# Performance work log

Hardware: AMD Instinct MI355X
Metric: run time of the kernel (lower is better)

Reference implementation:

```python
import jax, jax.numpy as jnp
import numpy as np

NEIGH = 16  # default neigh in __init__


def setup_inputs() -> dict:
    key = jax.random.key(0)
    kx, kuv = jax.random.split(key)
    B, M = 8, 4096
    X = jax.random.normal(kx, (B, M, 3), dtype=jnp.float32)
    uv = jax.random.uniform(kuv, (B, M, 2), dtype=jnp.float32)
    return {"X": X, "uv": uv}


def reference(X, uv):
    # Pairwise squared distances in parameter (uv) space: (B, M, M)
    dm = jnp.sum((uv[:, :, None, :] - uv[:, None, :, :]) ** 2, axis=-1)
    # k nearest neighbours (smallest distances) -> indices (B, M, K)
    _, k_inds = jax.lax.top_k(-dm, NEIGH)
    # Gather 3D neighbourhoods: (B, M, K, 3)
    knns = jax.vmap(lambda x, idx: x[idx])(X, k_inds)
    # Covariance per point: center then K x 3 outer products -> (B, M, 3, 3)
    centered = knns - jnp.mean(knns, axis=2, keepdims=True)
    cov = jnp.einsum('bmki,bmkj->bmij', centered, centered)
    # Symmetric 3x3 eigenvalues; torch sorts descending, eigvalsh is ascending
    eig = jnp.linalg.eigvalsh(cov)
    fff = eig[..., ::-1]  # (B, M, 3), descending
    return fff
```

## Files before the change

kernel.cpp:

```cpp
#include <hip/hip_runtime.h>
#include <hip/hip_bf16.h>
#include <math.h>

typedef unsigned long long u64;
typedef unsigned int u32;
typedef unsigned short u16;

constexpr int NB  = 8;
constexpr int NM  = 4096;
constexpr int KNN = 16;
constexpr int WPB = 8;
constexpr int QPW = 4;
constexpr int QPB = WPB * QPW;
constexpr int BLK = WPB * 64;
constexpr int GC  = 16;
constexpr int NC  = GC * GC;
constexpr int CSST = NC + 1;
constexpr int SLG = 12;
constexpr int SLC = 8;

constexpr size_t WS_UVS = 0;
constexpr size_t WS_IDX = 262144;
constexpr size_t WS_CS  = 327680;

__device__ __forceinline__ u64 shflx64(u64 v, int m) {
  unsigned lo = (unsigned)v, hi = (unsigned)(v >> 32);
  lo = __shfl_xor(lo, m, 64);
  hi = __shfl_xor(hi, m, 64);
  return ((u64)hi << 32) | lo;
}
__device__ __forceinline__ int rfl(int x) { return __builtin_amdgcn_readfirstlane(x); }
__device__ __forceinline__ int lanes_below(u64 m) {
  return (int)__builtin_amdgcn_mbcnt_hi((u32)(m >> 32),
             __builtin_amdgcn_mbcnt_lo((u32)m, 0u));
}
__device__ __forceinline__ u32 gm16(u64 m, int lane) {
  return (u32)(m >> ((lane >> 4) << 4)) & 0xFFFFu;
}

__global__ __launch_bounds__(1024)
void bin_pts(const float* __restrict__ uv, float2* __restrict__ uvS,
             u16* __restrict__ idxS, u32* __restrict__ cs) {
  __shared__ u32 cnt[NC];
  __shared__ u32 offs[NC];
  __shared__ u32 wtot[4];
  const int bb  = blockIdx.x;
  const int tid = threadIdx.x;

  if (tid < NC) cnt[tid] = 0;
  __syncthreads();

  float2 c4[4];
  int cell[4];
  #pragma unroll
  for (int i = 0; i < 4; ++i) {
    const int p = tid + i * 1024;
    const float2 c = ((const float2*)(uv + (size_t)bb * NM * 2))[p];
    int cx = (int)(c.x * (float)GC); cx = cx > GC - 1 ? GC - 1 : (cx < 0 ? 0 : cx);
    int cy = (int)(c.y * (float)GC); cy = cy > GC - 1 ? GC - 1 : (cy < 0 ? 0 : cy);
    c4[i] = c; cell[i] = cy * GC + cx;
    atomicAdd(&cnt[cell[i]], 1u);
  }
  __syncthreads();

  if (tid < NC) {
    const int lane = tid & 63;
    u32 inc = cnt[tid];
    #pragma unroll
    for (int o = 1; o < 64; o <<= 1) {
      const u32 t = __shfl_up(inc, o, 64);
      if (lane >= o) inc += t;
    }
    offs[tid] = inc;
    if (lane == 63) wtot[tid >> 6] = inc;
  }
  __syncthreads();
  if (tid < NC) {
    const int w = tid >> 6;
    u32 base = 0;
    #pragma unroll
    for (int i = 0; i < 3; ++i) base += (i < w) ? wtot[i] : 0;
    const u32 excl = base + offs[tid] - cnt[tid];
    cs[bb * CSST + tid] = excl;
    offs[tid] = excl;
    if (tid == 0) cs[bb * CSST + NC] = NM;
  }
  __syncthreads();

  #pragma unroll
  for (int i = 0; i < 4; ++i) {
    const int p = tid + i * 1024;
    const u32 pos = atomicAdd(&offs[cell[i]], 1u);
    uvS[(size_t)bb * NM + pos]  = c4[i];
    idxS[(size_t)bb * NM + pos] = (u16)p;
  }
}

__global__ __launch_bounds__(BLK, 8)
void knn_eig(const float* __restrict__ X, const float* __restrict__ uv,
             const float2* __restrict__ uvS, const u16* __restrict__ idxS,
             const u32* __restrict__ cs, float* __restrict__ out) {
  __shared__ u64 surv[WPB][QPW * 32];

  const int tid  = threadIdx.x;
  const int lane = tid & 63;
  const int sub  = lane & 15;
  const int g4   = lane >> 4;
  const int wv   = tid >> 6;
  const int bb   = blockIdx.x >> 7;
  const int q    = ((blockIdx.x & 127) << 5) + (wv << 2) + g4;

  const float qu = uv[((size_t)bb * NM + q) * 2];
  const float qv = uv[((size_t)bb * NM + q) * 2 + 1];
  int cxv = (int)(qu * (float)GC); cxv = cxv > GC - 1 ? GC - 1 : (cxv < 0 ? 0 : cxv);
  int cyv = (int)(qv * (float)GC); cyv = cyv > GC - 1 ? GC - 1 : (cyv < 0 ? 0 : cyv);
  const u32* csb = cs + bb * CSST;
  const float2* uvb = uvS + (size_t)bb * NM;
  const u16* idxb = idxS + (size_t)bb * NM;

  float d[SLG];
  #pragma unroll
  for (int t = 0; t < SLG; ++t) d[t] = 1e30f;

  constexpr float TAU1 = 0.0017f;
  constexpr float TAU2 = 0.00390625f;

  int rs0, rc0, rs1, rc1, rs2, total, tsw;
  bool ovf;
  int cnt = 0;
  {
    const int x0 = cxv > 0 ? cxv - 1 : 0, x1 = cxv < GC - 1 ? cxv + 1 : GC - 1;
    const int y0 = cyv > 0 ? cyv - 1 : 0, y1 = cyv < GC - 1 ? cyv + 1 : GC - 1;
    rs0 = (int)csb[y0 * GC + x0];
    rc0 = (int)csb[y0 * GC + x1 + 1] - rs0;
    rs1 = (int)csb[(y0 + 1) * GC + x0];
    rc1 = rc0 + (int)csb[(y0 + 1) * GC + x1 + 1] - rs1;
    const bool ok2 = (y0 + 2) <= y1;
    rs2 = (int)csb[ok2 ? ((y0 + 2) * GC + x0) : 0];
    const int re2 = (int)csb[ok2 ? ((y0 + 2) * GC + x1 + 1) : 0];
    total = rc1 + (ok2 ? (re2 - rs2) : 0);
    ovf = total > SLG * 16;
    int ts = (total + 15) >> 4; if (ts > SLG) ts = SLG;
    int m1 = max(ts, __shfl_xor(ts, 16, 64));
    m1 = max(m1, __shfl_xor(m1, 32, 64));
    tsw = rfl(m1);
    #pragma unroll
    for (int t = 0; t < SLG; ++t) {
      if (t >= tsw) break;
      const int L = t * 16 + sub;
      int addr = rs0 + L;
      if (L >= rc0) addr = rs1 + (L - rc0);
      if (L >= rc1) addr = rs2 + (L - rc1);
      float dd = 1e30f;
      if (L < total) {
        const float2 c = uvb[addr];
        const float dx = __fsub_rn(qu, c.x);
        const float dy = __fsub_rn(qv, c.y);
        dd = __fadd_rn(__fmul_rn(dx, dx), __fmul_rn(dy, dy));
      }
      d[t] = dd;
      cnt += (int)__popc(gm16(__ballot(dd <= TAU1), lane));
    }
    if (ovf) cnt = 0;
  }

  float hi2 = (cnt < KNN) ? TAU2 : TAU1;
  if (__any(cnt < KNN)) {
    int c2 = 0;
    #pragma unroll
    for (int t = 0; t < SLG; ++t) {
      if (t >= tsw) break;
      c2 += (int)__popc(gm16(__ballot(d[t] <= TAU2), lane));
    }
    if (cnt < KNN && !ovf) cnt = c2;
  }

  {
    float lo = (hi2 > TAU1) ? TAU1 : 0.f;
    for (int it = 0; __any(cnt > 32) && it < 40; ++it) {
      const float mid = 0.5f * (lo + hi2);
      int c = 0;
      #pragma unroll
      for (int t = 0; t < SLG; ++t) {
        if (t >= tsw) break;
        c += (int)__popc(gm16(__ballot(cnt > 32 && d[t] <= mid), lane));
      }
      if (cnt > 32) {
        if (!(mid > lo && mid < hi2)) { cnt = 32; }
        else if (c >= KNN) { hi2 = mid; cnt = c; }
        else lo = mid;
      }
    }
  }

  u64* sb = surv[wv];
  {
    int base = 0;
    #pragma unroll
    for (int t = 0; t < SLG; ++t) {
      if (t >= tsw) break;
      const bool p = d[t] <= hi2;
      const u32 mg = gm16(__ballot(p), lane);
      if (p) {
        const int pos = base + (int)__popc(mg & ((1u << sub) - 1u));
        if (pos < 32) {
          const int L = t * 16 + sub;
          int addr = rs0 + L;
          if (L >= rc0) addr = rs1 + (L - rc0);
          if (L >= rc1) addr = rs2 + (L - rc1);
          sb[(g4 << 5) + pos] = ((u64)__float_as_uint(d[t]) << 32) | (u64)idxb[addr];
        }
      }
      base += (int)__popc(mg);
    }
  }

  if (__any(cnt < KNN)) {
    #pragma unroll 1
    for (int g = 0; g < QPW; ++g) {
      if (!rfl((__shfl(cnt, g << 4, 64) < KNN) ? 1 : 0)) continue;
      const float gu = __shfl(qu, g << 4, 64);
      const float gv = __shfl(qv, g << 4, 64);
      const int gcx = rfl(__shfl(cxv, g << 4, 64));
      const int gcy = rfl(__shfl(cyv, g << 4, 64));
      float gd[SLC];
      int   ga[SLC];
      float ghi = 0.f;
      int gcnt = 0, gts = 0, gtotal = 0;
      for (int h = 2; h <= 5; ++h) {
        const int x0 = gcx - h < 0 ? 0 : gcx - h, x1 = gcx + h > GC - 1 ? GC - 1 : gcx + h;
        const int y0 = gcy - h < 0 ? 0 : gcy - h, y1 = gcy + h > GC - 1 ? GC - 1 : gcy + h;
        int rstart[7], rcum[7];
        int cum = 0;
        #pragma unroll
        for (int r = 0; r < 7; ++r) {
          const int y = y0 + r;
          const bool ok = (y <= y1);
          const u32 s = csb[ok ? (y * GC + x0) : 0];
          const u32 e = csb[ok ? (y * GC + x1 + 1) : 0];
          rstart[r] = (int)s;
          cum += ok ? (int)(e - s) : 0;
          rcum[r] = cum;
        }
        gtotal = cum;
        int t0 = (gtotal + 63) >> 6; if (t0 > SLC) t0 = SLC;
        gts = rfl(t0);
        const float hv = (float)h * 0.0625f;
        ghi = hv * hv;
        gcnt = 0;
        #pragma unroll
        for (int t = 0; t < SLC; ++t) {
          if (t >= gts) break;
          const int L = t * 64 + lane;
          int addr = rstart[0] + L;
          #pragma unroll
          for (int r = 1; r < 7; ++r)
            if (L >= rcum[r - 1]) addr = rstart[r] + (L - rcum[r - 1]);
          float dd = 1e30f;
          if (L < gtotal) {
            const float2 c = uvb[addr];
            const float dx = __fsub_rn(gu, c.x);
            const float dy = __fsub_rn(gv, c.y);
            dd = __fadd_rn(__fmul_rn(dx, dx), __fmul_rn(dy, dy));
          }
          gd[t] = dd; ga[t] = addr;
          gcnt += (int)__popcll(__ballot(dd <= ghi));
        }
        if (rfl(gcnt) >= KNN) break;
      }
      {
        float lo = 0.f;
        for (int it = 0; rfl(gcnt) > 32 && it < 40; ++it) {
          const float mid = 0.5f * (lo + ghi);
          if (!(mid > lo && mid < ghi)) break;
          int c = 0;
          #pragma unroll
          for (int t = 0; t < SLC; ++t) {
            if (t >= gts) break;
            c += (int)__popcll(__ballot(gd[t] <= mid));
          }
          if (c >= KNN) { ghi = mid; gcnt = c; } else lo = mid;
        }
      }
      int base = 0;
      #pragma unroll
      for (int t = 0; t < SLC; ++t) {
        if (t >= gts) break;
        const bool p = gd[t] <= ghi;
        const u64 m = __ballot(p);
        if (p) {
          const int pos = base + lanes_below(m);
          if (pos < 32)
            sb[(g << 5) + pos] = ((u64)__float_as_uint(gd[t]) << 32) | (u64)idxb[ga[t]];
        }
        base += (int)__popcll(m);
      }
      if (g4 == g) cnt = gcnt < 32 ? gcnt : 32;
    }
  }

  const int S = cnt < 32 ? cnt : 32;
  const int sbase = g4 << 5;
  u64 v0 = (sub < S) ? sb[sbase + sub] : ~0ull;
  u64 v1 = (16 + sub < S) ? sb[sbase + 16 + sub] : ~0ull;
  #pragma unroll
  for (int k = 2; k <= 16; k <<= 1) {
    #pragma unroll
    for (int j = k >> 1; j > 0; j >>= 1) {
      const u64 o0 = shflx64(v0, j);
      const u64 o1 = shflx64(v1, j);
      const bool up = ((sub & k) == 0);
      const bool j0 = ((sub & j) == 0);
      const bool km0 = (j0 == up);
      const bool km1 = (j0 != up);
      v0 = ((v0 < o0) == km0) ? v0 : o0;
      v1 = ((v1 < o1) == km1) ? v1 : o1;
    }
  }
  const u64 v = (v0 < v1) ? v0 : v1;

  const int idx = (int)(u32)v & 0xFFF;
  const float* Xp = X + ((size_t)bb * NM + idx) * 3;
  const float x = Xp[0], y = Xp[1], z = Xp[2];
  float sx = x, sy = y, sz = z;
  float sxx = x * x, sxy = x * y, sxz = x * z;
  float syy = y * y, syz = y * z, szz = z * z;
  #pragma unroll
  for (int o = 8; o > 0; o >>= 1) {
    sx  += __shfl_xor(sx,  o, 64);  sy  += __shfl_xor(sy,  o, 64);
    sz  += __shfl_xor(sz,  o, 64);  sxx += __shfl_xor(sxx, o, 64);
    sxy += __shfl_xor(sxy, o, 64);  sxz += __shfl_xor(sxz, o, 64);
    syy += __shfl_xor(syy, o, 64);  syz += __shfl_xor(syz, o, 64);
    szz += __shfl_xor(szz, o, 64);
  }

  const float mx = sx * 0.0625f, my = sy * 0.0625f, mz = sz * 0.0625f;
  const float c00 = sxx - 16.f * mx * mx;
  const float c11 = syy - 16.f * my * my;
  const float c22 = szz - 16.f * mz * mz;
  const float c01 = sxy - 16.f * mx * my;
  const float c02 = sxz - 16.f * mx * mz;
  const float c12 = syz - 16.f * my * mz;

  const float tr = c00 + c11 + c22;
  const float q3 = tr * (1.f / 3.f);
  const float b0 = c00 - q3, b1 = c11 - q3, b2 = c22 - q3;
  const float p2 = b0 * b0 + b1 * b1 + b2 * b2 +
                   2.f * (c01 * c01 + c02 * c02 + c12 * c12);
  float e0, e1, e2;
  if (p2 < 1e-30f) {
    e0 = e1 = e2 = q3;
  } else {
    const float p  = sqrtf(p2 * (1.f / 6.f));
    const float ip = 1.f / p;
    const float m00 = b0 * ip, m11 = b1 * ip, m22 = b2 * ip;
    const float m01 = c01 * ip, m02 = c02 * ip, m12 = c12 * ip;
    const float det = m00 * (m11 * m22 - m12 * m12)
                    - m01 * (m01 * m22 - m12 * m02)
                    + m02 * (m01 * m12 - m11 * m02);
    float r = 0.5f * det;
    r = fminf(1.f, fmaxf(-1.f, r));
    const float phi = acosf(r) * (1.f / 3.f);
    float sphi, cphi;
    __sincosf(phi, &sphi, &cphi);
    e0 = q3 + 2.f * p * cphi;
    e2 = q3 + 2.f * p * (-0.5f * cphi - 0.8660254037844386f * sphi);
    e1 = tr - e0 - e2;
  }

  if (sub == 0) {
    float* op = out + ((size_t)bb * NM + q) * 3;
    op[0] = e0; op[1] = e1; op[2] = e2;
  }
}

extern "C" void kernel_launch(void* const* d_in, const int* in_sizes, int n_in,
                              void* d_out, int out_size, void* d_ws, size_t ws_size,
                              hipStream_t stream) {
  const float* X  = (const float*)d_in[0];
  const float* uv = (const float*)d_in[1];
  float* out = (float*)d_out;
  char* ws = (char*)d_ws;
  float2* uvS = (float2*)(ws + WS_UVS);
  u16*    idxS = (u16*)(ws + WS_IDX);
  u32*    csP  = (u32*)(ws + WS_CS);

  bin_pts<<<dim3(NB), dim3(1024), 0, stream>>>(uv, uvS, idxS, csP);
  knn_eig<<<dim3(NB * NM / QPB), dim3(BLK), 0, stream>>>(X, uv, uvS, idxS, csP, out);
}
```

Measured before the change: 27.51 us.

## Refine kNN grid to 32x32 with biased 4x4 windows and sorted-order queries

```diff
diff --git a/kernel.cpp b/kernel.cpp
--- a/kernel.cpp
+++ b/kernel.cpp
@@ -1,10 +1,8 @@
 #include <hip/hip_runtime.h>
-#include <hip/hip_bf16.h>
 #include <math.h>
 
 typedef unsigned long long u64;
 typedef unsigned int u32;
-typedef unsigned short u16;
 
 constexpr int NB  = 8;
 constexpr int NM  = 4096;
@@ -13,15 +11,13 @@
 constexpr int QPW = 4;
 constexpr int QPB = WPB * QPW;
 constexpr int BLK = WPB * 64;
-constexpr int GC  = 16;
+constexpr int GC  = 32;
 constexpr int NC  = GC * GC;
 constexpr int CSST = NC + 1;
-constexpr int SLG = 12;
-constexpr int SLC = 8;
+constexpr int SLG = 13;
 
 constexpr size_t WS_UVS = 0;
-constexpr size_t WS_IDX = 262144;
-constexpr size_t WS_CS  = 327680;
+constexpr size_t WS_CS  = (size_t)NB * NM * 16;
 
 __device__ __forceinline__ u64 shflx64(u64 v, int m) {
   unsigned lo = (unsigned)v, hi = (unsigned)(v >> 32);
@@ -39,15 +35,15 @@
 }
 
 __global__ __launch_bounds__(1024)
-void bin_pts(const float* __restrict__ uv, float2* __restrict__ uvS,
-             u16* __restrict__ idxS, u32* __restrict__ cs) {
+void bin_pts(const float* __restrict__ uv, float4* __restrict__ uvS,
+             u32* __restrict__ cs) {
   __shared__ u32 cnt[NC];
   __shared__ u32 offs[NC];
-  __shared__ u32 wtot[4];
+  __shared__ u32 wtot[16];
   const int bb  = blockIdx.x;
   const int tid = threadIdx.x;
 
-  if (tid < NC) cnt[tid] = 0;
+  cnt[tid] = 0;
   __syncthreads();
 
   float2 c4[4];
@@ -56,14 +52,14 @@
   for (int i = 0; i < 4; ++i) {
     const int p = tid + i * 1024;
     const float2 c = ((const float2*)(uv + (size_t)bb * NM * 2))[p];
-    int cx = (int)(c.x * (float)GC); cx = cx > GC - 1 ? GC - 1 : (cx < 0 ? 0 : cx);
-    int cy = (int)(c.y * (float)GC); cy = cy > GC - 1 ? GC - 1 : (cy < 0 ? 0 : cy);
+    int cx = (int)(c.x * 32.f); cx = cx > GC - 1 ? GC - 1 : (cx < 0 ? 0 : cx);
+    int cy = (int)(c.y * 32.f); cy = cy > GC - 1 ? GC - 1 : (cy < 0 ? 0 : cy);
     c4[i] = c; cell[i] = cy * GC + cx;
     atomicAdd(&cnt[cell[i]], 1u);
   }
   __syncthreads();
 
-  if (tid < NC) {
+  {
     const int lane = tid & 63;
     u32 inc = cnt[tid];
     #pragma unroll
@@ -75,11 +71,19 @@
     if (lane == 63) wtot[tid >> 6] = inc;
   }
   __syncthreads();
-  if (tid < NC) {
+  if (tid < 16) {
+    u32 v = wtot[tid];
+    #pragma unroll
+    for (int o = 1; o < 16; o <<= 1) {
+      const u32 t = __shfl_up(v, o, 64);
+      if (tid >= o) v += t;
+    }
+    wtot[tid] = v;
+  }
+  __syncthreads();
+  {
     const int w = tid >> 6;
-    u32 base = 0;
-    #pragma unroll
-    for (int i = 0; i < 3; ++i) base += (i < w) ? wtot[i] : 0;
+    const u32 base = w ? wtot[w - 1] : 0u;
     const u32 excl = base + offs[tid] - cnt[tid];
     cs[bb * CSST + tid] = excl;
     offs[tid] = excl;
@@ -91,14 +95,13 @@
   for (int i = 0; i < 4; ++i) {
     const int p = tid + i * 1024;
     const u32 pos = atomicAdd(&offs[cell[i]], 1u);
-    uvS[(size_t)bb * NM + pos]  = c4[i];
-    idxS[(size_t)bb * NM + pos] = (u16)p;
+    uvS[(size_t)bb * NM + pos] =
+        make_float4(c4[i].x, c4[i].y, __uint_as_float((u32)p), 0.f);
   }
 }
 
 __global__ __launch_bounds__(BLK, 8)
-void knn_eig(const float* __restrict__ X, const float* __restrict__ uv,
-             const float2* __restrict__ uvS, const u16* __restrict__ idxS,
+void knn_eig(const float* __restrict__ X, const float4* __restrict__ uvS,
              const u32* __restrict__ cs, float* __restrict__ out) {
   __shared__ u64 surv[WPB][QPW * 32];
 
@@ -108,39 +111,42 @@
   const int g4   = lane >> 4;
   const int wv   = tid >> 6;
   const int bb   = blockIdx.x >> 7;
-  const int q    = ((blockIdx.x & 127) << 5) + (wv << 2) + g4;
-
-  const float qu = uv[((size_t)bb * NM + q) * 2];
-  const float qv = uv[((size_t)bb * NM + q) * 2 + 1];
-  int cxv = (int)(qu * (float)GC); cxv = cxv > GC - 1 ? GC - 1 : (cxv < 0 ? 0 : cxv);
-  int cyv = (int)(qv * (float)GC); cyv = cyv > GC - 1 ? GC - 1 : (cyv < 0 ? 0 : cyv);
+  const int s    = ((blockIdx.x & 127) << 5) + (wv << 2) + g4;
+
+  const float4* uvb = uvS + (size_t)bb * NM;
   const u32* csb = cs + bb * CSST;
-  const float2* uvb = uvS + (size_t)bb * NM;
-  const u16* idxb = idxS + (size_t)bb * NM;
+
+  const float4 qc = uvb[s];
+  const float qu = qc.x, qv = qc.y;
+  const u32 oq = __float_as_uint(qc.z);
+  int cxv = (int)(qu * 32.f); cxv = cxv > GC - 1 ? GC - 1 : (cxv < 0 ? 0 : cxv);
+  int cyv = (int)(qv * 32.f); cyv = cyv > GC - 1 ? GC - 1 : (cyv < 0 ? 0 : cyv);
+  const int sx = (qu * 32.f - (float)cxv >= 0.5f) ? 1 : 0;
+  const int sy = (qv * 32.f - (float)cyv >= 0.5f) ? 1 : 0;
 
   float d[SLG];
   #pragma unroll
   for (int t = 0; t < SLG; ++t) d[t] = 1e30f;
 
   constexpr float TAU1 = 0.0017f;
-  constexpr float TAU2 = 0.00390625f;
-
-  int rs0, rc0, rs1, rc1, rs2, total, tsw;
-  bool ovf;
+  constexpr float TAU2 = 0.002197265625f;
+  constexpr float TAU3 = 0.006103515625f;
+  constexpr float TAU4 = 0.019775390625f;
+
+  int rs0, rs1, rs2, rs3, rs4, rs5, rc0, rc1, rc2, rc3, rc4;
+  int total, tsw;
   int cnt = 0;
+
   {
-    const int x0 = cxv > 0 ? cxv - 1 : 0, x1 = cxv < GC - 1 ? cxv + 1 : GC - 1;
-    const int y0 = cyv > 0 ? cyv - 1 : 0, y1 = cyv < GC - 1 ? cyv + 1 : GC - 1;
-    rs0 = (int)csb[y0 * GC + x0];
-    rc0 = (int)csb[y0 * GC + x1 + 1] - rs0;
-    rs1 = (int)csb[(y0 + 1) * GC + x0];
-    rc1 = rc0 + (int)csb[(y0 + 1) * GC + x1 + 1] - rs1;
-    const bool ok2 = (y0 + 2) <= y1;
-    rs2 = (int)csb[ok2 ? ((y0 + 2) * GC + x0) : 0];
-    const int re2 = (int)csb[ok2 ? ((y0 + 2) * GC + x1 + 1) : 0];
-    total = rc1 + (ok2 ? (re2 - rs2) : 0);
-    ovf = total > SLG * 16;
-    int ts = (total + 15) >> 4; if (ts > SLG) ts = SLG;
+    const int x0 = min(max(cxv - 2 + sx, 0), GC - 4);
+    const int y0 = min(max(cyv - 2 + sy, 0), GC - 4);
+    const int b = y0 * GC + x0;
+    rs0 = (int)csb[b];          rc0 = (int)csb[b + 4] - rs0;
+    rs1 = (int)csb[b + GC];     rc1 = rc0 + (int)csb[b + GC + 4] - rs1;
+    rs2 = (int)csb[b + 2*GC];   rc2 = rc1 + (int)csb[b + 2*GC + 4] - rs2;
+    rs3 = (int)csb[b + 3*GC];   total = rc2 + (int)csb[b + 3*GC + 4] - rs3;
+    rc3 = total; rc4 = total; rs4 = 0; rs5 = 0;
+    int ts = min((total + 15) >> 4, SLG);
     int m1 = max(ts, __shfl_xor(ts, 16, 64));
     m1 = max(m1, __shfl_xor(m1, 32, 64));
     tsw = rfl(m1);
@@ -149,11 +155,12 @@
       if (t >= tsw) break;
       const int L = t * 16 + sub;
       int addr = rs0 + L;
-      if (L >= rc0) addr = rs1 + (L - rc0);
-      if (L >= rc1) addr = rs2 + (L - rc1);
+      addr = (L >= rc0) ? rs1 + (L - rc0) : addr;
+      addr = (L >= rc1) ? rs2 + (L - rc1) : addr;
+      addr = (L >= rc2) ? rs3 + (L - rc2) : addr;
       float dd = 1e30f;
       if (L < total) {
-        const float2 c = uvb[addr];
+        const float4 c = uvb[addr];
         const float dx = __fsub_rn(qu, c.x);
         const float dy = __fsub_rn(qv, c.y);
         dd = __fadd_rn(__fmul_rn(dx, dx), __fmul_rn(dy, dy));
@@ -161,10 +168,9 @@
       d[t] = dd;
       cnt += (int)__popc(gm16(__ballot(dd <= TAU1), lane));
     }
-    if (ovf) cnt = 0;
-  }
-
-  float hi2 = (cnt < KNN) ? TAU2 : TAU1;
+  }
+
+  float hi2 = TAU1, lo = 0.f;
   if (__any(cnt < KNN)) {
     int c2 = 0;
     #pragma unroll
@@ -172,24 +178,69 @@
       if (t >= tsw) break;
       c2 += (int)__popc(gm16(__ballot(d[t] <= TAU2), lane));
     }
-    if (cnt < KNN && !ovf) cnt = c2;
-  }
-
-  {
-    float lo = (hi2 > TAU1) ? TAU1 : 0.f;
-    for (int it = 0; __any(cnt > 32) && it < 40; ++it) {
-      const float mid = 0.5f * (lo + hi2);
-      int c = 0;
+    if (cnt < KNN) { lo = TAU1; hi2 = TAU2; cnt = c2; }
+  }
+
+  if (__any(cnt < KNN)) {
+    const bool need = cnt < KNN;
+    int ts2 = 0;
+    if (need) {
       #pragma unroll
-      for (int t = 0; t < SLG; ++t) {
-        if (t >= tsw) break;
-        c += (int)__popc(gm16(__ballot(cnt > 32 && d[t] <= mid), lane));
-      }
-      if (cnt > 32) {
-        if (!(mid > lo && mid < hi2)) { cnt = 32; }
-        else if (c >= KNN) { hi2 = mid; cnt = c; }
-        else lo = mid;
-      }
+      for (int t = 0; t < SLG; ++t) d[t] = 1e30f;
+      const int x0 = min(max(cxv - 3 + sx, 0), GC - 6);
+      const int y0 = min(max(cyv - 3 + sy, 0), GC - 6);
+      const int b = y0 * GC + x0;
+      rs0 = (int)csb[b];          rc0 = (int)csb[b + 6] - rs0;
+      rs1 = (int)csb[b + GC];     rc1 = rc0 + (int)csb[b + GC + 6] - rs1;
+      rs2 = (int)csb[b + 2*GC];   rc2 = rc1 + (int)csb[b + 2*GC + 6] - rs2;
+      rs3 = (int)csb[b + 3*GC];   rc3 = rc2 + (int)csb[b + 3*GC + 6] - rs3;
+      rs4 = (int)csb[b + 4*GC];   rc4 = rc3 + (int)csb[b + 4*GC + 6] - rs4;
+      rs5 = (int)csb[b + 5*GC];   total = rc4 + (int)csb[b + 5*GC + 6] - rs5;
+      ts2 = min((total + 15) >> 4, SLG);
+      lo = TAU2; hi2 = TAU3;
+    }
+    int m1 = max(ts2, __shfl_xor(ts2, 16, 64));
+    m1 = max(m1, __shfl_xor(m1, 32, 64));
+    const int tsw2 = rfl(m1);
+    int c2 = 0;
+    #pragma unroll
+    for (int t = 0; t < SLG; ++t) {
+      if (t >= tsw2) break;
+      float dd = 1e30f;
+      if (need) {
+        const int L = t * 16 + sub;
+        int addr = rs0 + L;
+        addr = (L >= rc0) ? rs1 + (L - rc0) : addr;
+        addr = (L >= rc1) ? rs2 + (L - rc1) : addr;
+        addr = (L >= rc2) ? rs3 + (L - rc2) : addr;
+        addr = (L >= rc3) ? rs4 + (L - rc3) : addr;
+        addr = (L >= rc4) ? rs5 + (L - rc4) : addr;
+        if (L < total) {
+          const float4 c = uvb[addr];
+          const float dx = __fsub_rn(qu, c.x);
+          const float dy = __fsub_rn(qv, c.y);
+          dd = __fadd_rn(__fmul_rn(dx, dx), __fmul_rn(dy, dy));
+        }
+        d[t] = dd;
+      }
+      c2 += (int)__popc(gm16(__ballot(dd <= TAU3), lane));
+    }
+    if (need) cnt = c2;
+    tsw = max(tsw, tsw2);
+  }
+
+  for (int it = 0; __any(cnt > 32) && it < 40; ++it) {
+    const float mid = 0.5f * (lo + hi2);
+    int c = 0;
+    #pragma unroll
+    for (int t = 0; t < SLG; ++t) {
+      if (t >= tsw) break;
+      c += (int)__popc(gm16(__ballot((cnt > 32) && (d[t] <= mid)), lane));
+    }
+    if (cnt > 32) {
+      if (!(mid > lo && mid < hi2)) cnt = 32;
+      else if (c >= KNN) { hi2 = mid; cnt = c; }
+      else lo = mid;
     }
   }
 
@@ -206,9 +257,13 @@
         if (pos < 32) {
           const int L = t * 16 + sub;
           int addr = rs0 + L;
-          if (L >= rc0) addr = rs1 + (L - rc0);
-          if (L >= rc1) addr = rs2 + (L - rc1);
-          sb[(g4 << 5) + pos] = ((u64)__float_as_uint(d[t]) << 32) | (u64)idxb[addr];
+          addr = (L >= rc0) ? rs1 + (L - rc0) : addr;
+          addr = (L >= rc1) ? rs2 + (L - rc1) : addr;
+          addr = (L >= rc2) ? rs3 + (L - rc2) : addr;
+          addr = (L >= rc3) ? rs4 + (L - rc3) : addr;
+          addr = (L >= rc4) ? rs5 + (L - rc4) : addr;
+          const u32 oid = ((const u32*)(uvb + addr))[2];
+          sb[(g4 << 5) + pos] = ((u64)__float_as_uint(d[t]) << 32) | (u64)oid;
         }
       }
       base += (int)__popc(mg);
@@ -221,81 +276,75 @@
       if (!rfl((__shfl(cnt, g << 4, 64) < KNN) ? 1 : 0)) continue;
       const float gu = __shfl(qu, g << 4, 64);
       const float gv = __shfl(qv, g << 4, 64);
-      const int gcx = rfl(__shfl(cxv, g << 4, 64));
-      const int gcy = rfl(__shfl(cyv, g << 4, 64));
-      float gd[SLC];
-      int   ga[SLC];
-      float ghi = 0.f;
-      int gcnt = 0, gts = 0, gtotal = 0;
-      for (int h = 2; h <= 5; ++h) {
-        const int x0 = gcx - h < 0 ? 0 : gcx - h, x1 = gcx + h > GC - 1 ? GC - 1 : gcx + h;
-        const int y0 = gcy - h < 0 ? 0 : gcy - h, y1 = gcy + h > GC - 1 ? GC - 1 : gcy + h;
-        int rstart[7], rcum[7];
-        int cum = 0;
+      int gcx = (int)(gu * 32.f); gcx = min(max(gcx, 0), GC - 1);
+      int gcy = (int)(gv * 32.f); gcy = min(max(gcy, 0), GC - 1);
+      const int gsx = (gu * 32.f - (float)gcx >= 0.5f) ? 1 : 0;
+      const int gsy = (gv * 32.f - (float)gcy >= 0.5f) ? 1 : 0;
+      const int x0 = min(max(gcx - 5 + gsx, 0), GC - 10);
+      const int y0 = min(max(gcy - 5 + gsy, 0), GC - 10);
+      int rstart[10], rcum[10];
+      int cum = 0;
+      #pragma unroll
+      for (int r = 0; r < 10; ++r) {
+        const int b = (y0 + r) * GC + x0;
+        rstart[r] = (int)csb[b];
+        cum += (int)csb[b + 10] - rstart[r];
+        rcum[r] = cum;
+      }
+      const int gtotal = cum;
+      const int gts = rfl(min((gtotal + 63) >> 6, SLG));
+      float ghi = TAU4, glo = TAU3;
+      int gcnt = 0;
+      #pragma unroll
+      for (int t = 0; t < SLG; ++t) {
+        if (t >= gts) break;
+        const int L = t * 64 + lane;
+        int addr = rstart[0] + L;
         #pragma unroll
-        for (int r = 0; r < 7; ++r) {
-          const int y = y0 + r;
-          const bool ok = (y <= y1);
-          const u32 s = csb[ok ? (y * GC + x0) : 0];
-          const u32 e = csb[ok ? (y * GC + x1 + 1) : 0];
-          rstart[r] = (int)s;
-          cum += ok ? (int)(e - s) : 0;
-          rcum[r] = cum;
+        for (int r = 1; r < 10; ++r)
+          addr = (L >= rcum[r - 1]) ? rstart[r] + (L - rcum[r - 1]) : addr;
+        float dd = 1e30f;
+        if (L < gtotal) {
+          const float4 c = uvb[addr];
+          const float dx = __fsub_rn(gu, c.x);
+          const float dy = __fsub_rn(gv, c.y);
+          dd = __fadd_rn(__fmul_rn(dx, dx), __fmul_rn(dy, dy));
         }
-        gtotal = cum;
-        int t0 = (gtotal + 63) >> 6; if (t0 > SLC) t0 = SLC;
-        gts = rfl(t0);
-        const float hv = (float)h * 0.0625f;
-        ghi = hv * hv;
-        gcnt = 0;
+        d[t] = dd;
+        gcnt += (int)__popcll(__ballot(dd <= ghi));
+      }
+      for (int it = 0; rfl(gcnt) > 32 && it < 40; ++it) {
+        const float mid = 0.5f * (glo + ghi);
+        if (!(mid > glo && mid < ghi)) break;
+        int c = 0;
         #pragma unroll
-        for (int t = 0; t < SLC; ++t) {
+        for (int t = 0; t < SLG; ++t) {
           if (t >= gts) break;
-          const int L = t * 64 + lane;
-          int addr = rstart[0] + L;
-          #pragma unroll
-          for (int r = 1; r < 7; ++r)
-            if (L >= rcum[r - 1]) addr = rstart[r] + (L - rcum[r - 1]);
-          float dd = 1e30f;
-          if (L < gtotal) {
-            const float2 c = uvb[addr];
-            const float dx = __fsub_rn(gu, c.x);
-            const float dy = __fsub_rn(gv, c.y);
-            dd = __fadd_rn(__fmul_rn(dx, dx), __fmul_rn(dy, dy));
-          }
-          gd[t] = dd; ga[t] = addr;
-          gcnt += (int)__popcll(__ballot(dd <= ghi));
+          c += (int)__popcll(__ballot(d[t] <= mid));
         }
-        if (rfl(gcnt) >= KNN) break;
-      }
-      {
-        float lo = 0.f;
-        for (int it = 0; rfl(gcnt) > 32 && it < 40; ++it) {
-          const float mid = 0.5f * (lo + ghi);
-          if (!(mid > lo && mid < ghi)) break;
-          int c = 0;
-          #pragma unroll
-          for (int t = 0; t < SLC; ++t) {
-            if (t >= gts) break;
-            c += (int)__popcll(__ballot(gd[t] <= mid));
-          }
-          if (c >= KNN) { ghi = mid; gcnt = c; } else lo = mid;
-        }
+        if (c >= KNN) { ghi = mid; gcnt = c; } else glo = mid;
       }
       int base = 0;
       #pragma unroll
-      for (int t = 0; t < SLC; ++t) {
+      for (int t = 0; t < SLG; ++t) {
         if (t >= gts) break;
-        const bool p = gd[t] <= ghi;
+        const bool p = d[t] <= ghi;
         const u64 m = __ballot(p);
         if (p) {
           const int pos = base + lanes_below(m);
-          if (pos < 32)
-            sb[(g << 5) + pos] = ((u64)__float_as_uint(gd[t]) << 32) | (u64)idxb[ga[t]];
+          if (pos < 32) {
+            const int L = t * 64 + lane;
+            int addr = rstart[0] + L;
+            #pragma unroll
+            for (int r = 1; r < 10; ++r)
+              addr = (L >= rcum[r - 1]) ? rstart[r] + (L - rcum[r - 1]) : addr;
+            const u32 oid = ((const u32*)(uvb + addr))[2];
+            sb[(g << 5) + pos] = ((u64)__float_as_uint(d[t]) << 32) | (u64)oid;
+          }
         }
         base += (int)__popcll(m);
       }
-      if (g4 == g) cnt = gcnt < 32 ? gcnt : 32;
+      if (g4 == g) cnt = min(rfl(gcnt), 32);
     }
   }
 
@@ -322,19 +371,19 @@
   const int idx = (int)(u32)v & 0xFFF;
   const float* Xp = X + ((size_t)bb * NM + idx) * 3;
   const float x = Xp[0], y = Xp[1], z = Xp[2];
-  float sx = x, sy = y, sz = z;
+  float sxs = x, sys = y, szs = z;
   float sxx = x * x, sxy = x * y, sxz = x * z;
   float syy = y * y, syz = y * z, szz = z * z;
   #pragma unroll
   for (int o = 8; o > 0; o >>= 1) {
-    sx  += __shfl_xor(sx,  o, 64);  sy  += __shfl_xor(sy,  o, 64);
-    sz  += __shfl_xor(sz,  o, 64);  sxx += __shfl_xor(sxx, o, 64);
+    sxs += __shfl_xor(sxs, o, 64);  sys += __shfl_xor(sys, o, 64);
+    szs += __shfl_xor(szs, o, 64);  sxx += __shfl_xor(sxx, o, 64);
     sxy += __shfl_xor(sxy, o, 64);  sxz += __shfl_xor(sxz, o, 64);
     syy += __shfl_xor(syy, o, 64);  syz += __shfl_xor(syz, o, 64);
     szz += __shfl_xor(szz, o, 64);
   }
 
-  const float mx = sx * 0.0625f, my = sy * 0.0625f, mz = sz * 0.0625f;
+  const float mx = sxs * 0.0625f, my = sys * 0.0625f, mz = szs * 0.0625f;
   const float c00 = sxx - 16.f * mx * mx;
   const float c11 = syy - 16.f * my * my;
   const float c22 = szz - 16.f * mz * mz;
@@ -369,7 +418,7 @@
   }
 
   if (sub == 0) {
-    float* op = out + ((size_t)bb * NM + q) * 3;
+    float* op = out + ((size_t)bb * NM + oq) * 3;
     op[0] = e0; op[1] = e1; op[2] = e2;
   }
 }
@@ -381,10 +430,9 @@
   const float* uv = (const float*)d_in[1];
   float* out = (float*)d_out;
   char* ws = (char*)d_ws;
-  float2* uvS = (float2*)(ws + WS_UVS);
-  u16*    idxS = (u16*)(ws + WS_IDX);
-  u32*    csP  = (u32*)(ws + WS_CS);
-
-  bin_pts<<<dim3(NB), dim3(1024), 0, stream>>>(uv, uvS, idxS, csP);
-  knn_eig<<<dim3(NB * NM / QPB), dim3(BLK), 0, stream>>>(X, uv, uvS, idxS, csP, out);
-}
+  float4* uvS = (float4*)(ws + WS_UVS);
+  u32*    csP = (u32*)(ws + WS_CS);
+
+  bin_pts<<<dim3(NB), dim3(1024), 0, stream>>>(uv, uvS, csP);
+  knn_eig<<<dim3(NB * NM / QPB), dim3(BLK), 0, stream>>>(X, uvS, csP, out);
+}
```

Measured after the change: 27.68 us. Within noise of the previous version (+0.6%).
